# Kernel optimization log

Hardware: AMD Instinct MI355X
Metric: run time of the kernel (lower is better)

## Reference

```python
import jax, jax.numpy as jnp
import numpy as np
import math

H = 1024      # hidden_size
NH = 16       # num_heads
HD = H // NH  # head_dim
MS = 256      # memory_size
MD = 512      # memory_dim
B, S = 2, 2048


def setup_inputs() -> dict:
    key = jax.random.key(0)
    ks = jax.random.split(key, 12)
    sd = 1.0 / math.sqrt(H)
    inp = {
        "hidden_states": jax.random.normal(ks[0], (B, S, H), dtype=jnp.float32),
        "attention_mask": jnp.zeros((B, S), dtype=jnp.float32),
        "Wq": jax.random.normal(ks[1], (H, H), dtype=jnp.float32) * sd,
        "bq": jnp.zeros((H,), dtype=jnp.float32),
        "Wk": jax.random.normal(ks[2], (H, H), dtype=jnp.float32) * sd,
        "bk": jnp.zeros((H,), dtype=jnp.float32),
        "Wv": jax.random.normal(ks[3], (H, H), dtype=jnp.float32) * sd,
        "bv": jnp.zeros((H,), dtype=jnp.float32),
        "Wo": jax.random.normal(ks[4], (H, H), dtype=jnp.float32) * sd,
        "bo": jnp.zeros((H,), dtype=jnp.float32),
        "memory_values": jax.random.normal(ks[5], (MS, MD), dtype=jnp.float32),
        "Wmp": jax.random.normal(ks[6], (H, MD), dtype=jnp.float32) * (1.0 / math.sqrt(MD)),
        "bmp": jnp.zeros((H,), dtype=jnp.float32),
        "Wma": jax.random.normal(ks[7], (MS, H), dtype=jnp.float32) * sd,
        "bma": jnp.zeros((MS,), dtype=jnp.float32),
    }
    return inp


def reference(hidden_states, attention_mask, Wq, bq, Wk, bk, Wv, bv, Wo, bo,
              memory_values, Wmp, bmp, Wma, bma):
    b, s, h = hidden_states.shape
    scale = math.sqrt(HD)
    # projections (nn.Linear: x @ W.T + b)
    q = hidden_states @ Wq.T + bq
    k = hidden_states @ Wk.T + bk
    v = hidden_states @ Wv.T + bv
    # [b, nh, s, hd]
    q = q.reshape(b, s, NH, HD).transpose(0, 2, 1, 3)
    k = k.reshape(b, s, NH, HD).transpose(0, 2, 1, 3)
    v = v.reshape(b, s, NH, HD).transpose(0, 2, 1, 3)
    # full score matrix [b, nh, s, s] (faithful to original naive MHA)
    attn_scores = jnp.einsum('bhqd,bhkd->bhqk', q, k) / scale
    attn_scores = attn_scores + attention_mask[:, None, None, :] * (-1e9)
    attn_probs = jax.nn.softmax(attn_scores, axis=-1)  # dropout = identity (eval)
    attn_output = jnp.einsum('bhqk,bhkd->bhqd', attn_probs, v)
    attn_output = attn_output.transpose(0, 2, 1, 3).reshape(b, s, h)
    # memory-bank cross attention
    mem_scores = hidden_states @ Wma.T + bma            # [b, s, MS]
    mem_probs = jax.nn.softmax(mem_scores, axis=-1)
    mem_out = mem_probs @ memory_values                  # [b, s, MD]
    mem_out = mem_out @ Wmp.T + bmp                      # [b, s, H]
    combined = attn_output + 0.3 * mem_out
    return combined @ Wo.T + bo
```

## Files before the change

### kernel.cpp

```cpp
#include <hip/hip_runtime.h>

typedef __bf16 bf16;
typedef __bf16 bf16x8 __attribute__((ext_vector_type(8)));
typedef __bf16 bf16x4 __attribute__((ext_vector_type(4)));
typedef float  f32x4  __attribute__((ext_vector_type(4)));
typedef float  f32x16 __attribute__((ext_vector_type(16)));
typedef unsigned u32x2 __attribute__((ext_vector_type(2)));
typedef unsigned u32x4 __attribute__((ext_vector_type(4)));
typedef unsigned long long uptr;

#define MFMA16(a, b, c) __builtin_amdgcn_mfma_f32_16x16x32_bf16((a), (b), (c), 0, 0, 0)
#define MFMA32(a, b, c) __builtin_amdgcn_mfma_f32_32x32x16_bf16((a), (b), (c), 0, 0, 0)

__device__ __forceinline__ void gl_lds16(const void* g, void* l) {
  __builtin_amdgcn_global_load_lds(
      (__attribute__((address_space(1))) void*)(uptr)(g),
      (__attribute__((address_space(3))) void*)(uptr)(l),
      16, 0, 0);
}
__device__ __forceinline__ void gl_lds4(const void* g, void* l) {
  __builtin_amdgcn_global_load_lds(
      (__attribute__((address_space(1))) void*)(uptr)(g),
      (__attribute__((address_space(3))) void*)(uptr)(l),
      4, 0, 0);
}
__device__ __forceinline__ unsigned cvtpk_bf16(float lo, float hi) {
  unsigned r;
  asm("v_cvt_pk_bf16_f32 %0, %1, %2" : "=v"(r) : "v"(lo), "v"(hi));
  return r;
}

__global__ __launch_bounds__(256) void fused_prep(
    const float* __restrict__ X, const float* __restrict__ Wq,
    const float* __restrict__ Wk, const float* __restrict__ Wv,
    const float* __restrict__ Wo, const float* __restrict__ Wma,
    const float* __restrict__ Wmp, const float* __restrict__ mask,
    const float* __restrict__ bq, const float* __restrict__ bk,
    const float* __restrict__ bv, const float* __restrict__ bma,
    const float* __restrict__ mv,
    bf16* __restrict__ Xb, bf16* __restrict__ Wqkvb, bf16* __restrict__ Wob,
    bf16* __restrict__ Wmpb,
    float* __restrict__ M2, float* __restrict__ bqkv, bf16* __restrict__ mvTb) {
  const int bid = blockIdx.x, t = threadIdx.x;
  const float QS = 0.125f * 1.44269504f;
  auto cvt = [&](const float* src, bf16* dst, int blk, float sc) {
    const long i = ((long)blk * 256 + t) * 4;
    const float4 v = *(const float4*)(src + i);
    bf16x4 o = {(bf16)(v.x * sc), (bf16)(v.y * sc), (bf16)(v.z * sc), (bf16)(v.w * sc)};
    *(bf16x4*)(dst + i) = o;
  };
  if (bid < 4096) cvt(X, Xb, bid, 1.0f);
  else if (bid < 5120) cvt(Wq, Wqkvb, bid - 4096, QS);
  else if (bid < 6144) cvt(Wk, Wqkvb + 1024 * 1024, bid - 5120, 1.0f);
  else if (bid < 7168) cvt(Wv, Wqkvb + 2 * 1024 * 1024, bid - 6144, 1.0f);
  else if (bid < 8192) cvt(Wo, Wob, bid - 7168, 1.0f);
  else if (bid < 8448) cvt(Wma, Wqkvb + 3072 * 1024, bid - 8192, 1.0f);
  else if (bid < 8960) cvt(Wmp, Wmpb, bid - 8448, 1.0f);
  else if (bid < 8964) {
    const long i = ((long)(bid - 8960) * 256 + t) * 4;
    const float4 v = *(const float4*)(mask + i);
    float4 o = {v.x * -1.44269504e9f - 40.0f, v.y * -1.44269504e9f - 40.0f,
                v.z * -1.44269504e9f - 40.0f, v.w * -1.44269504e9f - 40.0f};
    *(float4*)(M2 + i) = o;
  } else if (bid < 8967) {
    const int s = bid - 8964;
    const float* src = s == 0 ? bq : (s == 1 ? bk : bv);
    const float sc = s == 0 ? QS : 1.0f;
    float4 v = *(const float4*)(src + t * 4);
    float4 o = {v.x * sc, v.y * sc, v.z * sc, v.w * sc};
    *(float4*)(bqkv + s * 1024 + t * 4) = o;
  } else if (bid < 8968) {
    if (t < 64) *(float4*)(bqkv + 3072 + t * 4) = *(const float4*)(bma + t * 4);
  } else {
    const int d = bid - 8968;
    mvTb[(long)d * 256 + t] = (bf16)mv[(long)t * 512 + d];
  }
}

__global__ __launch_bounds__(256) void softmax_rows256(const float* __restrict__ in,
                                                       bf16* __restrict__ out) {
  const int w = threadIdx.x >> 6, l = threadIdx.x & 63;
  const long row = (long)blockIdx.x * 4 + w;
  const float4 v = *(const float4*)(in + row * 256 + l * 4);
  float mx = fmaxf(fmaxf(v.x, v.y), fmaxf(v.z, v.w));
  mx = fmaxf(mx, __shfl_xor(mx, 1, 64));
  mx = fmaxf(mx, __shfl_xor(mx, 2, 64));
  mx = fmaxf(mx, __shfl_xor(mx, 4, 64));
  mx = fmaxf(mx, __shfl_xor(mx, 8, 64));
  mx = fmaxf(mx, __shfl_xor(mx, 16, 64));
  mx = fmaxf(mx, __shfl_xor(mx, 32, 64));
  const float e0 = __expf(v.x - mx), e1 = __expf(v.y - mx);
  const float e2 = __expf(v.z - mx), e3 = __expf(v.w - mx);
  float sm = e0 + e1 + e2 + e3;
  sm += __shfl_xor(sm, 1, 64);
  sm += __shfl_xor(sm, 2, 64);
  sm += __shfl_xor(sm, 4, 64);
  sm += __shfl_xor(sm, 8, 64);
  sm += __shfl_xor(sm, 16, 64);
  sm += __shfl_xor(sm, 32, 64);
  const float inv = 1.0f / sm;
  bf16x4 o = {(bf16)(e0 * inv), (bf16)(e1 * inv), (bf16)(e2 * inv), (bf16)(e3 * inv)};
  *(bf16x4*)(out + row * 256 + l * 4) = o;
}

template <typename OutT, bool COMBINE>
__global__ __launch_bounds__(256, 3) void gemm_bt(
    const bf16* __restrict__ A, const bf16* __restrict__ B,
    const float* __restrict__ bias, const bf16* __restrict__ Op,
    const float* __restrict__ mlp, OutT* __restrict__ C,
    int M, int N, int K, float alpha) {
  __shared__ bf16 lA[2][128 * 64];
  __shared__ bf16 lB[2][64 * 64];
  const int tid = threadIdx.x;
  const int w = tid >> 6, l = tid & 63;
  const int hi = l >> 4, lo = l & 15;
  const int m0 = blockIdx.y * 128, n0 = blockIdx.x * 64;
  const int wm = w * 32;

  const int sr8 = l >> 3;
  const int sc = (l & 7) * 8;
  const long aRow = (long)(m0 + wm + sr8);
  const long bRow = (long)(n0 + w * 16 + sr8);

  auto stage = [&](int p, int k0) {
#pragma unroll
    for (int j = 0; j < 4; ++j)
      gl_lds16(A + (aRow + 8 * j) * K + k0 + sc, (char*)lA[p] + (wm + 8 * j) * 128);
#pragma unroll
    for (int j = 0; j < 2; ++j)
      gl_lds16(B + (bRow + 8 * j) * K + k0 + sc, (char*)lB[p] + (w * 16 + 8 * j) * 128);
  };

  f32x4 acc[2][4] = {};
  stage(0, 0);
  __syncthreads();
  const int nt = K >> 6;

  for (int t = 0; t < nt; ++t) {
    const int p = t & 1;
    if (t + 1 < nt) stage(p ^ 1, (t + 1) << 6);
#pragma unroll
    for (int kk = 0; kk < 2; ++kk) {
      bf16x8 af[2], bfr[4];
#pragma unroll
      for (int mi = 0; mi < 2; ++mi)
        af[mi] = *(const bf16x8*)((const char*)lA[p] + (wm + mi * 16 + lo) * 128 + kk * 64 + hi * 16);
#pragma unroll
      for (int ni = 0; ni < 4; ++ni)
        bfr[ni] = *(const bf16x8*)((const char*)lB[p] + (ni * 16 + lo) * 128 + kk * 64 + hi * 16);
      __builtin_amdgcn_s_setprio(1);
#pragma unroll
      for (int mi = 0; mi < 2; ++mi)
#pragma unroll
        for (int ni = 0; ni < 4; ++ni)
          acc[mi][ni] = MFMA16(af[mi], bfr[ni], acc[mi][ni]);
      __builtin_amdgcn_s_setprio(0);
    }
    __syncthreads();
  }

#pragma unroll
  for (int ni = 0; ni < 4; ++ni) {
    const int col = n0 + ni * 16 + lo;
    const float bv = bias ? bias[col] : 0.0f;
#pragma unroll
    for (int mi = 0; mi < 2; ++mi) {
      const int mrow = m0 + wm + mi * 16 + hi * 4;
#pragma unroll
      for (int r = 0; r < 4; ++r) {
        const long row = mrow + r;
        float v = (acc[mi][ni][r] + bv) * alpha;
        if (COMBINE) {
          const int h = col >> 6;
          const float l0 = mlp[row * 16 + h];
          const float l1 = mlp[(4096L + row) * 16 + h];
          const float o0v = (float)Op[row * 1024 + col];
          const float o1v = (float)Op[4096L * 1024 + row * 1024 + col];
          v += (o0v + o1v) / (l0 + l1);
        }
        C[row * (long)N + col] = (OutT)v;
      }
    }
  }
}

__global__ __launch_bounds__(256, 3) void gemm_qkv(
    const bf16* __restrict__ A, const bf16* __restrict__ B,
    const float* __restrict__ bias, bf16* __restrict__ Qo,
    bf16* __restrict__ Ko, bf16* __restrict__ Vto, float* __restrict__ MSc) {
  const int K = 1024;
  __shared__ bf16 smem[2][128 * 64];
  bf16* lA = smem[0];
  bf16* lB = smem[1];
  const int tid = threadIdx.x;
  const int w = tid >> 6, l = tid & 63;
  const int hi = l >> 4, lo = l & 15;
  const int m0 = blockIdx.y * 128, n0 = blockIdx.x * 128;
  const int wm = (w >> 1) * 64, wn = (w & 1) * 64;

  const int sr = w * 32 + (l >> 3);
  const int sc = (l & 7) * 8;
  const long aBase = (long)(m0 + sr) * K + sc;
  const long bBase = (long)(n0 + sr) * K + sc;

  f32x4 acc[4][4] = {};

  for (int k0 = 0; k0 < K; k0 += 64) {
#pragma unroll
    for (int j = 0; j < 4; ++j) {
      gl_lds16(A + aBase + (long)8 * j * K + k0, (char*)lA + (w * 32 + 8 * j) * 128);
      gl_lds16(B + bBase + (long)8 * j * K + k0, (char*)lB + (w * 32 + 8 * j) * 128);
    }
    __syncthreads();
#pragma unroll
    for (int kk = 0; kk < 2; ++kk) {
      bf16x8 af[4], bfr[4];
#pragma unroll
      for (int i = 0; i < 4; ++i) {
        af[i]  = *(const bf16x8*)((const char*)lA + (wm + i * 16 + lo) * 128 + kk * 64 + hi * 16);
        bfr[i] = *(const bf16x8*)((const char*)lB + (wn + i * 16 + lo) * 128 + kk * 64 + hi * 16);
      }
#pragma unroll
      for (int mi = 0; mi < 4; ++mi)
#pragma unroll
        for (int ni = 0; ni < 4; ++ni)
          acc[mi][ni] = MFMA16(af[mi], bfr[ni], acc[mi][ni]);
    }
    __syncthreads();
  }

  if (n0 < 2048) {
#pragma unroll
    for (int ni = 0; ni < 4; ++ni) {
      const int col = n0 + wn + ni * 16 + lo;
      const float bv = bias[col];
#pragma unroll
      for (int mi = 0; mi < 4; ++mi) {
        const int mrow = m0 + wm + mi * 16 + hi * 4;
#pragma unroll
        for (int r = 0; r < 4; ++r) {
          const long row = mrow + r;
          const float v = acc[mi][ni][r] + bv;
          if (n0 < 1024) Qo[row * 1024 + col] = (bf16)v;
          else           Ko[row * 1024 + (col - 1024)] = (bf16)v;
        }
      }
    }
  } else if (n0 < 3072) {
    bf16* sT = smem[0];
#pragma unroll
    for (int ni = 0; ni < 4; ++ni) {
      const int cT = wn + ni * 16 + lo;
      const float bv = bias[n0 + cT];
#pragma unroll
      for (int mi = 0; mi < 4; ++mi) {
        const int rT = wm + mi * 16 + hi * 4;
        u32x2 pw = {cvtpk_bf16(acc[mi][ni][0] + bv, acc[mi][ni][1] + bv),
                    cvtpk_bf16(acc[mi][ni][2] + bv, acc[mi][ni][3] + bv)};
        *(u32x2*)((char*)sT + cT * 256 + ((rT * 2) ^ ((cT & 15) << 3))) = pw;
      }
    }
    __syncthreads();
    const long vrow0 = (long)(m0 >> 11) * 1024 + (n0 - 2048);
    const int srow = m0 & 2047;
#pragma unroll
    for (int dd = 0; dd < 32; ++dd) {
      const int d = w * 32 + dd;
      const unsigned pv = *(const unsigned*)((const char*)sT + d * 256 + ((l * 4) ^ ((d & 15) << 3)));
      *(unsigned*)((char*)(Vto + (vrow0 + d) * 2048 + srow) + l * 4) = pv;
    }
  } else {
#pragma unroll
    for (int ni = 0; ni < 4; ++ni) {
      const int col = n0 + wn + ni * 16 + lo;
      const float bv = bias[col];
      const int cm = col - 3072;
#pragma unroll
      for (int mi = 0; mi < 4; ++mi) {
        const int mrow = m0 + wm + mi * 16 + hi * 4;
#pragma unroll
        for (int r = 0; r < 4; ++r)
          MSc[(long)(mrow + r) * 256 + cm] = acc[mi][ni][r] + bv;
      }
    }
  }
}

__global__ __launch_bounds__(256, 4) void attn_fwd(
    const bf16* __restrict__ Q, const bf16* __restrict__ Km,
    const bf16* __restrict__ Vt, const float* __restrict__ M2,
    bf16* __restrict__ Opart, float* __restrict__ ml) {
  __shared__ bf16 lK[2][64 * 64];
  __shared__ bf16 lV[2][64 * 64];
  __shared__ alignas(16) float lM[2][64];
  const int tid = threadIdx.x, w = tid >> 6, l = tid & 63;
  const int q31 = l & 31, h32 = l >> 5;
  const int b = blockIdx.z >> 1, half = blockIdx.z & 1;
  const int hh = blockIdx.y, q0 = blockIdx.x * 128;
  const long S = 2048, H = 1024;
  const int kbase = half * 1024;

  bf16x8 qf[4];
  const long qrow = (long)b * S + q0 + w * 32 + q31;
#pragma unroll
  for (int sl = 0; sl < 4; ++sl)
    qf[sl] = *(const bf16x8*)(Q + qrow * H + hh * 64 + sl * 16 + h32 * 8);

  f32x16 o0 = {}, o1 = {};
  float lrun = 0.0f;

  const int swr = w * 16 + (l >> 3);
  const int swc = ((l & 7) ^ (l >> 3)) * 8;

  auto stage = [&](int p, int k0) {
#pragma unroll
    for (int j = 0; j < 2; ++j) {
      gl_lds16(Km + ((long)b * S + k0 + swr + 8 * j) * H + hh * 64 + swc,
               (char*)lK[p] + (w * 16 + 8 * j) * 128);
      gl_lds16(Vt + ((long)b * H + hh * 64 + swr + 8 * j) * S + k0 + swc,
               (char*)lV[p] + (w * 16 + 8 * j) * 128);
    }
    if (w == 0) gl_lds4(M2 + (long)b * S + k0 + l, (char*)lM[p]);
  };

  stage(0, kbase);
  __syncthreads();

  for (int t = 0; t < 16; ++t) {
    const int p = t & 1;
    if (t < 15) stage(p ^ 1, kbase + (t + 1) * 64);

    f32x16 s0, s1;
#pragma unroll
    for (int g = 0; g < 4; ++g) {
      const f32x4 m0 = *(const f32x4*)&lM[p][8 * g + 4 * h32];
      const f32x4 m1 = *(const f32x4*)&lM[p][32 + 8 * g + 4 * h32];
#pragma unroll
      for (int r = 0; r < 4; ++r) {
        s0[4 * g + r] = m0[r];
        s1[4 * g + r] = m1[r];
      }
    }

    __builtin_amdgcn_s_setprio(1);
#pragma unroll
    for (int sl = 0; sl < 4; ++sl) {
      const int ch = sl * 2 + h32;
      const int cx = (ch ^ (q31 & 7)) * 16;
      const bf16x8 k0f = *(const bf16x8*)((const char*)lK[p] + q31 * 128 + cx);
      const bf16x8 k1f = *(const bf16x8*)((const char*)lK[p] + (32 + q31) * 128 + cx);
      s0 = MFMA32(k0f, qf[sl], s0);
      s1 = MFMA32(k1f, qf[sl], s1);
    }
    __builtin_amdgcn_s_setprio(0);

#pragma unroll
    for (int i = 0; i < 16; ++i) s0[i] = __builtin_amdgcn_exp2f(s0[i]);
#pragma unroll
    for (int i = 0; i < 16; ++i) s1[i] = __builtin_amdgcn_exp2f(s1[i]);

    f32x16 ts;
#pragma unroll
    for (int i = 0; i < 16; ++i) ts[i] = s0[i] + s1[i];
#pragma unroll
    for (int i = 0; i < 8; ++i) ts[i] += ts[i + 8];
#pragma unroll
    for (int i = 0; i < 4; ++i) ts[i] += ts[i + 4];
    float rs = (ts[0] + ts[1]) + (ts[2] + ts[3]);
    rs += __shfl_xor(rs, 32, 64);
    lrun += rs;

    bf16x8 pa[4];
#pragma unroll
    for (int ks = 0; ks < 4; ++ks) {
      const int rb = (ks & 1) * 8;
      unsigned a0, a1, b0, b1;
      if (ks < 2) {
        a0 = cvtpk_bf16(s0[rb + 0], s0[rb + 1]);
        a1 = cvtpk_bf16(s0[rb + 2], s0[rb + 3]);
        b0 = cvtpk_bf16(s0[rb + 4], s0[rb + 5]);
        b1 = cvtpk_bf16(s0[rb + 6], s0[rb + 7]);
      } else {
        a0 = cvtpk_bf16(s1[rb + 0], s1[rb + 1]);
        a1 = cvtpk_bf16(s1[rb + 2], s1[rb + 3]);
        b0 = cvtpk_bf16(s1[rb + 4], s1[rb + 5]);
        b1 = cvtpk_bf16(s1[rb + 6], s1[rb + 7]);
      }
      const u32x2 r02 = __builtin_amdgcn_permlane32_swap(a0, b0, false, false);
      const u32x2 r13 = __builtin_amdgcn_permlane32_swap(a1, b1, false, false);
      const u32x4 pw = {r02[0], r13[0], r02[1], r13[1]};
      pa[ks] = __builtin_bit_cast(bf16x8, pw);
    }

    __builtin_amdgcn_s_setprio(1);
#pragma unroll
    for (int ks = 0; ks < 4; ++ks) {
      const int ch = ks * 2 + h32;
      const int cx = (ch ^ (q31 & 7)) * 16;
      const bf16x8 v0 = *(const bf16x8*)((const char*)lV[p] + q31 * 128 + cx);
      const bf16x8 v1 = *(const bf16x8*)((const char*)lV[p] + (32 + q31) * 128 + cx);
      o0 = MFMA32(pa[ks], v0, o0);
      o1 = MFMA32(pa[ks], v1, o1);
    }
    __builtin_amdgcn_s_setprio(0);
    __syncthreads();
  }

  if (h32 == 0)
    ml[((long)half * 4096 + (long)b * 2048 + q0 + w * 32 + q31) * 16 + hh] = lrun;
#pragma unroll
  for (int reg = 0; reg < 16; ++reg) {
    const int row = (reg & 3) + 8 * (reg >> 2) + 4 * h32;
    const long qg = (long)b * 2048 + q0 + w * 32 + row;
    Opart[((long)half * 4096 + qg) * 1024 + hh * 64 + q31]      = (bf16)o0[reg];
    Opart[((long)half * 4096 + qg) * 1024 + hh * 64 + 32 + q31] = (bf16)o1[reg];
  }
}

extern "C" void kernel_launch(void* const* d_in, const int* in_sizes, int n_in,
                              void* d_out, int out_size, void* d_ws, size_t ws_size,
                              hipStream_t stream) {
  const float* X    = (const float*)d_in[0];
  const float* mask = (const float*)d_in[1];
  const float* Wq   = (const float*)d_in[2];  const float* bq  = (const float*)d_in[3];
  const float* Wk   = (const float*)d_in[4];  const float* bk  = (const float*)d_in[5];
  const float* Wv   = (const float*)d_in[6];  const float* bv  = (const float*)d_in[7];
  const float* Wo   = (const float*)d_in[8];  const float* bo  = (const float*)d_in[9];
  const float* mv   = (const float*)d_in[10];
  const float* Wmp  = (const float*)d_in[11]; const float* bmp = (const float*)d_in[12];
  const float* Wma  = (const float*)d_in[13]; const float* bma = (const float*)d_in[14];

  char* ws = (char*)d_ws;
  size_t off = 0;
  auto alloc = [&](size_t bytes) -> void* {
    void* p = ws + off;
    off += (bytes + 255) & ~(size_t)255;
    return p;
  };
  const long MS_ = 4096;
  bf16* Xb    = (bf16*)alloc(MS_ * 1024 * 2);
  bf16* Wqkvb = (bf16*)alloc(3328L * 1024 * 2);
  bf16* Wob   = (bf16*)alloc(1024 * 1024 * 2);
  bf16* Wmpb  = (bf16*)alloc(1024 * 512 * 2);
  bf16* mvTb  = (bf16*)alloc(512 * 256 * 2);
  float* M2   = (float*)alloc(MS_ * 4);
  float* bqkv = (float*)alloc(3328 * 4);
  bf16* Qb    = (bf16*)alloc(MS_ * 1024 * 2);
  bf16* Kb    = (bf16*)alloc(MS_ * 1024 * 2);
  bf16* Vtb   = (bf16*)alloc(MS_ * 1024 * 2);
  bf16* Opart = (bf16*)alloc(2 * MS_ * 1024 * 2);
  float* ml   = (float*)alloc(2 * MS_ * 16 * 4);
  float* MSc  = (float*)alloc(MS_ * 256 * 4);
  bf16* MP    = (bf16*)alloc(MS_ * 256 * 2);
  bf16* MO    = Kb;
  bf16* CB    = Qb;

  fused_prep<<<9480, 256, 0, stream>>>(X, Wq, Wk, Wv, Wo, Wma, Wmp, mask,
                                       bq, bk, bv, bma, mv,
                                       Xb, Wqkvb, Wob, Wmpb, M2, bqkv, mvTb);
  gemm_qkv<<<dim3(26, 32), 256, 0, stream>>>(Xb, Wqkvb, bqkv, Qb, Kb, Vtb, MSc);
  attn_fwd<<<dim3(16, 16, 4), 256, 0, stream>>>(Qb, Kb, Vtb, M2, Opart, ml);
  softmax_rows256<<<1024, 256, 0, stream>>>(MSc, MP);
  gemm_bt<bf16, false><<<dim3(8, 32), 256, 0, stream>>>(MP, mvTb, nullptr, nullptr, nullptr,
                                                        MO, 4096, 512, 256, 1.0f);
  gemm_bt<bf16, true><<<dim3(16, 32), 256, 0, stream>>>(MO, Wmpb, bmp, Opart, ml,
                                                        CB, 4096, 1024, 512, 0.3f);
  gemm_bt<float, false><<<dim3(16, 32), 256, 0, stream>>>(CB, Wob, bo, nullptr, nullptr,
                                                          (float*)d_out, 4096, 1024, 1024, 1.0f);
}
```

Measured before the change: 140.0 us.

## Restructure QKV GEMM to 256x256 tiles with double-buffered swizzled LDS pipeline

The fused QKV+memory-score GEMM now uses 512-thread blocks with 256x256 output tiles and a 1D grid of 208 blocks, remapped so that blocks sharing an N-tile are spread across XCDs. K-tiles are double-buffered in 128KB of LDS with an XOR-swizzled layout, explicit vmcnt/lgkmcnt waits and raw barriers, plus s_setprio around the MFMA bursts. The aim is more operand reuse per LDS load, fewer bank conflicts and overlap of global loads with compute. In exchange it uses far more registers and LDS per block, so occupancy drops to at most one or two blocks per CU, and 208 blocks may leave part of the GPU underfilled.

```diff
diff --git a/kernel.cpp b/kernel.cpp
--- a/kernel.cpp
+++ b/kernel.cpp
@@ -184,103 +184,137 @@
   }
 }
 
-__global__ __launch_bounds__(256, 3) void gemm_qkv(
+__global__ __launch_bounds__(512, 2) void gemm_qkv(
     const bf16* __restrict__ A, const bf16* __restrict__ B,
     const float* __restrict__ bias, bf16* __restrict__ Qo,
     bf16* __restrict__ Ko, bf16* __restrict__ Vto, float* __restrict__ MSc) {
   const int K = 1024;
-  __shared__ bf16 smem[2][128 * 64];
-  bf16* lA = smem[0];
-  bf16* lB = smem[1];
-  const int tid = threadIdx.x;
-  const int w = tid >> 6, l = tid & 63;
+  __shared__ char sm[131072];
+  const int lin = blockIdx.x;
+  const int role = (lin & 7) * 26 + (lin >> 3);
+  const int mt = role & 15, ntile = role >> 4;
+  const int m0 = mt * 256, n0 = ntile * 256;
+  const int tid = threadIdx.x, wid = tid >> 6, l = tid & 63;
   const int hi = l >> 4, lo = l & 15;
-  const int m0 = blockIdx.y * 128, n0 = blockIdx.x * 128;
-  const int wm = (w >> 1) * 64, wn = (w & 1) * 64;
-
-  const int sr = w * 32 + (l >> 3);
-  const int sc = (l & 7) * 8;
-  const long aBase = (long)(m0 + sr) * K + sc;
-  const long bBase = (long)(n0 + sr) * K + sc;
-
-  f32x4 acc[4][4] = {};
-
-  for (int k0 = 0; k0 < K; k0 += 64) {
-#pragma unroll
-    for (int j = 0; j < 4; ++j) {
-      gl_lds16(A + aBase + (long)8 * j * K + k0, (char*)lA + (w * 32 + 8 * j) * 128);
-      gl_lds16(B + bBase + (long)8 * j * K + k0, (char*)lB + (w * 32 + 8 * j) * 128);
-    }
-    __syncthreads();
+  const int wm = (wid >> 2) * 128;
+  const int wn = (wid & 3) * 64;
+
+  const int srow = wid * 8 + (l >> 3);
+  const int schk = ((l & 7) ^ (l >> 3)) * 8;
+
+  auto STAGE = [&](int p, int kt) {
+    const int k0 = kt << 6;
+    char* dA = sm + p * 65536;
+    char* dB = dA + 32768;
+#pragma unroll
+    for (int j = 0; j < 4; ++j)
+      gl_lds16(A + (long)(m0 + j * 64 + srow) * K + k0 + schk, dA + j * 8192 + wid * 1024);
+#pragma unroll
+    for (int j = 0; j < 4; ++j)
+      gl_lds16(B + (long)(n0 + j * 64 + srow) * K + k0 + schk, dB + j * 8192 + wid * 1024);
+  };
+
+  f32x4 acc[8][4] = {};
+
+  STAGE(0, 0);
+  STAGE(1, 1);
+  asm volatile("s_waitcnt vmcnt(8)" ::: "memory");
+  __builtin_amdgcn_s_barrier();
+  __builtin_amdgcn_sched_barrier(0);
+
+  for (int t = 0; t < 16; ++t) {
+    const char* bA = sm + (t & 1) * 65536;
+    const char* bB = bA + 32768;
 #pragma unroll
     for (int kk = 0; kk < 2; ++kk) {
-      bf16x8 af[4], bfr[4];
-#pragma unroll
-      for (int i = 0; i < 4; ++i) {
-        af[i]  = *(const bf16x8*)((const char*)lA + (wm + i * 16 + lo) * 128 + kk * 64 + hi * 16);
-        bfr[i] = *(const bf16x8*)((const char*)lB + (wn + i * 16 + lo) * 128 + kk * 64 + hi * 16);
-      }
-#pragma unroll
-      for (int mi = 0; mi < 4; ++mi)
-#pragma unroll
-        for (int ni = 0; ni < 4; ++ni)
-          acc[mi][ni] = MFMA16(af[mi], bfr[ni], acc[mi][ni]);
-    }
-    __syncthreads();
+      const int cx = ((kk * 4 + hi) ^ (lo & 7)) * 16;
+      bf16x8 af[8], bfr[4];
+#pragma unroll
+      for (int mf = 0; mf < 8; ++mf)
+        af[mf] = *(const bf16x8*)(bA + (wm + mf * 16 + lo) * 128 + cx);
+#pragma unroll
+      for (int nf = 0; nf < 4; ++nf)
+        bfr[nf] = *(const bf16x8*)(bB + (wn + nf * 16 + lo) * 128 + cx);
+      __builtin_amdgcn_s_setprio(1);
+#pragma unroll
+      for (int mf = 0; mf < 8; ++mf)
+#pragma unroll
+        for (int nf = 0; nf < 4; ++nf)
+          acc[mf][nf] = MFMA16(af[mf], bfr[nf], acc[mf][nf]);
+      __builtin_amdgcn_s_setprio(0);
+    }
+    if (t == 15) break;
+    asm volatile("s_waitcnt lgkmcnt(0)" ::: "memory");
+    __builtin_amdgcn_sched_barrier(0);
+    __builtin_amdgcn_s_barrier();
+    __builtin_amdgcn_sched_barrier(0);
+    if (t < 14) {
+      STAGE(t & 1, t + 2);
+      asm volatile("s_waitcnt vmcnt(8)" ::: "memory");
+    } else {
+      asm volatile("s_waitcnt vmcnt(0)" ::: "memory");
+    }
+    __builtin_amdgcn_s_barrier();
+    __builtin_amdgcn_sched_barrier(0);
   }
 
   if (n0 < 2048) {
 #pragma unroll
-    for (int ni = 0; ni < 4; ++ni) {
-      const int col = n0 + wn + ni * 16 + lo;
+    for (int nf = 0; nf < 4; ++nf) {
+      const int col = n0 + wn + nf * 16 + lo;
       const float bv = bias[col];
 #pragma unroll
-      for (int mi = 0; mi < 4; ++mi) {
-        const int mrow = m0 + wm + mi * 16 + hi * 4;
+      for (int mf = 0; mf < 8; ++mf) {
+        const int mrow = m0 + wm + mf * 16 + hi * 4;
 #pragma unroll
         for (int r = 0; r < 4; ++r) {
           const long row = mrow + r;
-          const float v = acc[mi][ni][r] + bv;
+          const float v = acc[mf][nf][r] + bv;
           if (n0 < 1024) Qo[row * 1024 + col] = (bf16)v;
           else           Ko[row * 1024 + (col - 1024)] = (bf16)v;
         }
       }
     }
-  } else if (n0 < 3072) {
-    bf16* sT = smem[0];
-#pragma unroll
-    for (int ni = 0; ni < 4; ++ni) {
-      const int cT = wn + ni * 16 + lo;
+  } else if (n0 >= 3072) {
+#pragma unroll
+    for (int nf = 0; nf < 4; ++nf) {
+      const int col = n0 + wn + nf * 16 + lo;
+      const float bv = bias[col];
+      const int cm = col - 3072;
+#pragma unroll
+      for (int mf = 0; mf < 8; ++mf) {
+        const int mrow = m0 + wm + mf * 16 + hi * 4;
+#pragma unroll
+        for (int r = 0; r < 4; ++r)
+          MSc[(long)(mrow + r) * 256 + cm] = acc[mf][nf][r] + bv;
+      }
+    }
+  } else {
+    asm volatile("s_waitcnt lgkmcnt(0)" ::: "memory");
+    __builtin_amdgcn_s_barrier();
+    char* sT = sm;
+#pragma unroll
+    for (int nf = 0; nf < 4; ++nf) {
+      const int cT = wn + nf * 16 + lo;
       const float bv = bias[n0 + cT];
 #pragma unroll
-      for (int mi = 0; mi < 4; ++mi) {
-        const int rT = wm + mi * 16 + hi * 4;
-        u32x2 pw = {cvtpk_bf16(acc[mi][ni][0] + bv, acc[mi][ni][1] + bv),
-                    cvtpk_bf16(acc[mi][ni][2] + bv, acc[mi][ni][3] + bv)};
-        *(u32x2*)((char*)sT + cT * 256 + ((rT * 2) ^ ((cT & 15) << 3))) = pw;
+      for (int mf = 0; mf < 8; ++mf) {
+        const int rT = wm + mf * 16 + hi * 4;
+        u32x2 pw = {cvtpk_bf16(acc[mf][nf][0] + bv, acc[mf][nf][1] + bv),
+                    cvtpk_bf16(acc[mf][nf][2] + bv, acc[mf][nf][3] + bv)};
+        *(u32x2*)(sT + cT * 512 + ((rT * 2) ^ ((cT & 15) << 3))) = pw;
       }
     }
     __syncthreads();
     const long vrow0 = (long)(m0 >> 11) * 1024 + (n0 - 2048);
-    const int srow = m0 & 2047;
+    const int scol = m0 & 2047;
 #pragma unroll
     for (int dd = 0; dd < 32; ++dd) {
-      const int d = w * 32 + dd;
-      const unsigned pv = *(const unsigned*)((const char*)sT + d * 256 + ((l * 4) ^ ((d & 15) << 3)));
-      *(unsigned*)((char*)(Vto + (vrow0 + d) * 2048 + srow) + l * 4) = pv;
-    }
-  } else {
-#pragma unroll
-    for (int ni = 0; ni < 4; ++ni) {
-      const int col = n0 + wn + ni * 16 + lo;
-      const float bv = bias[col];
-      const int cm = col - 3072;
-#pragma unroll
-      for (int mi = 0; mi < 4; ++mi) {
-        const int mrow = m0 + wm + mi * 16 + hi * 4;
-#pragma unroll
-        for (int r = 0; r < 4; ++r)
-          MSc[(long)(mrow + r) * 256 + cm] = acc[mi][ni][r] + bv;
+      const int d = wid * 32 + dd;
+#pragma unroll
+      for (int rr = 0; rr < 2; ++rr) {
+        const unsigned pv = *(const unsigned*)(sT + d * 512 + rr * 256 + ((l * 4) ^ ((d & 15) << 3)));
+        *(unsigned*)((char*)(Vto + (vrow0 + d) * 2048 + scol) + rr * 256 + l * 4) = pv;
       }
     }
   }
@@ -458,7 +492,7 @@
   fused_prep<<<9480, 256, 0, stream>>>(X, Wq, Wk, Wv, Wo, Wma, Wmp, mask,
                                        bq, bk, bv, bma, mv,
                                        Xb, Wqkvb, Wob, Wmpb, M2, bqkv, mvTb);
-  gemm_qkv<<<dim3(26, 32), 256, 0, stream>>>(Xb, Wqkvb, bqkv, Qb, Kb, Vtb, MSc);
+  gemm_qkv<<<208, 512, 0, stream>>>(Xb, Wqkvb, bqkv, Qb, Kb, Vtb, MSc);
   attn_fwd<<<dim3(16, 16, 4), 256, 0, stream>>>(Qb, Kb, Vtb, M2, Opart, ml);
   softmax_rows256<<<1024, 256, 0, stream>>>(MSc, MP);
   gemm_bt<bf16, false><<<dim3(8, 32), 256, 0, stream>>>(MP, mvTb, nullptr, nullptr, nullptr,
```

Measured after the change: 136.7 us. 1.02x faster.
